# Kernel tuning notes

Hardware: AMD Instinct MI355X
Metric: run time of the kernel (lower is better)

Reference implementation:

```python
import jax, jax.numpy as jnp
import numpy as np

N = 27          # number of graph nodes (hardcoded in the module)
NH = 28         # n_hidden = out_features = self_size + 1
H = 8192        # n_heads
HA = 256        # num_hiddens_action
NO = 5          # num_outputs_action


def setup_inputs() -> dict:
    key = jax.random.key(0)
    ks = jax.random.split(key, 8)
    # node_embeddings: one_hot(node, 27) ++ reward flag (reward_nodes=[2] -> node index 1)
    node_emb = jnp.concatenate(
        [jnp.eye(N, dtype=jnp.float32),
         (jnp.arange(N) == 1).astype(jnp.float32)[:, None]], axis=1)  # [27,28]
    # adjacency [27,27,1], 0/1 ints, self-loops forced so softmax columns are valid
    adj = (jax.random.uniform(ks[0], (N, N, 1)) < 0.3).astype(jnp.int32)
    adj = adj.at[jnp.arange(N), jnp.arange(N), 0].set(1)
    # obs: one-hot current-location vector, node index 5 -> cur_node = 6
    obs = jnp.zeros((1, N), dtype=jnp.float32).at[0, 5].set(1.0)
    s = 0.02
    W_lin = jax.random.normal(ks[1], (N + 1, NH * H), dtype=jnp.float32) * s
    W_attn = jax.random.normal(ks[2], (2 * NH, 1), dtype=jnp.float32) * s
    b_attn = jax.random.normal(ks[3], (1,), dtype=jnp.float32) * s
    W1 = jax.random.normal(ks[4], (N + 1, HA), dtype=jnp.float32) * s
    b1 = jax.random.normal(ks[5], (HA,), dtype=jnp.float32) * s
    W2 = jax.random.normal(ks[6], (HA, NO), dtype=jnp.float32) * s
    b2 = jax.random.normal(ks[7], (NO,), dtype=jnp.float32) * s
    return {"obs": obs, "node_emb": node_emb, "adj": adj, "W_lin": W_lin,
            "W_attn": W_attn, "b_attn": b_attn, "W1": W1, "b1": b1,
            "W2": W2, "b2": b2}


def _leaky(x, slope):
    return jnp.where(x >= 0, x, slope * x)


def reference(obs, node_emb, adj, W_lin, W_attn, b_attn, W1, b1, W2, b2):
    # per-head projection: [27,28] @ [28, 28*8192] -> [27, H, NH]
    g = (node_emb @ W_lin).reshape(N, H, NH)
    # attn(concat(g_i, g_j)) decomposed: e[i,j,h] = g_i.Wl + g_j.Wr + b
    # (mathematically identical to the repeat/repeat_interleave + concat path,
    #  avoids materializing the [27,27,H,2*NH] tensor)
    Wl = W_attn[:NH, 0]
    Wr = W_attn[NH:, 0]
    s_i = jnp.einsum('nhf,f->nh', g, Wl)  # [N,H]
    s_j = jnp.einsum('nhf,f->nh', g, Wr)  # [N,H]
    e = _leaky(s_i[:, None, :] + s_j[None, :, :] + b_attn[0], 0.2)  # [N,N,H]
    # mask non-edges; adj [N,N,1] broadcasts over heads
    e = jnp.where(adj == 0, -jnp.inf, e)
    # torch nn.Softmax() with no dim resolves to dim=0 for 3-D input
    a = jax.nn.softmax(e, axis=0)
    # dropout is identity in eval mode
    attn_res = jnp.einsum('ijh,jhf->ihf', a, g)  # [N,H,NH]
    attn_res = attn_res.mean(axis=1)             # is_concat=False -> [N,NH]
    # cur_node = get_loc(bool obs) + 1; select attn_res[cur_node-1]
    idx = jnp.argmax(obs[0] != 0)
    x = attn_res[idx]                            # [NH]
    h = _leaky(x @ W1 + b1, 0.01)                # default LeakyReLU slope
    return h @ W2 + b2                           # [NO]
```

## Files before the change

### kernel.cpp

```cpp
#include <hip/hip_runtime.h>
#include <math.h>

#define NN 27
#define KD 28
#define HD 8192
#define HA_ 256
#define NO_ 5
#define NPAIR (KD*HD)
#define HB 32
#define NBLK (HD/HB)

__global__ void __launch_bounds__(256) kMain(const float* __restrict__ obs,
                                             const int* __restrict__ adj,
                                             const float* __restrict__ Wlin,
                                             const float* __restrict__ Wattn,
                                             const float* __restrict__ battn,
                                             float* __restrict__ ws) {
    __shared__ float P[HB][KD + 1];
    __shared__ float Q[HB][KD + 1];
    __shared__ float A[HB][KD];
    __shared__ unsigned adjm[NN];
    __shared__ float red[4][KD];

    const int t   = threadIdx.x;
    const int hl  = t >> 3;
    const int sub = t & 7;
    const int h   = blockIdx.x * HB + hl;

    if (t < NN) {
        unsigned m = 0;
        for (int i = 0; i < NN; ++i) m |= (adj[i * NN + t] != 0 ? 1u : 0u) << i;
        adjm[t] = m;
    }

    float wl[KD], wr[KD];
#pragma unroll
    for (int f = 0; f < KD; ++f) { wl[f] = Wattn[f]; wr[f] = Wattn[KD + f]; }

#pragma unroll
    for (int m = 0; m < 4; ++m) {
        int k = sub + 8 * m;
        if (k < KD) {
            const float4* w4 = reinterpret_cast<const float4*>(
                Wlin + (size_t)k * NPAIR + (size_t)h * KD);
            float p = 0.f, q = 0.f;
#pragma unroll
            for (int f4 = 0; f4 < 7; ++f4) {
                float4 w = w4[f4];
                p += w.x * wl[4*f4] + w.y * wl[4*f4+1] + w.z * wl[4*f4+2] + w.w * wl[4*f4+3];
                q += w.x * wr[4*f4] + w.y * wr[4*f4+1] + w.z * wr[4*f4+2] + w.w * wr[4*f4+3];
            }
            P[hl][k] = p;
            Q[hl][k] = q;
        }
    }
    __syncthreads();

    int idx = 0;
    for (int n = NN - 1; n >= 0; --n) if (obs[n] != 0.f) idx = n;
    const float bias = battn[0];

    float si[NN];
#pragma unroll
    for (int i = 0; i < NN; ++i)
        si[i] = P[hl][i] + (i == 1 ? P[hl][27] : 0.f) + bias;

#pragma unroll
    for (int m = 0; m < 4; ++m) {
        int j = sub + 8 * m;
        if (j < NN) {
            float sj = Q[hl][j] + (j == 1 ? Q[hl][27] : 0.f);
            unsigned msk = adjm[j];
            float ev[NN];
            float mx = -3.0e38f;
#pragma unroll
            for (int i = 0; i < NN; ++i) {
                float e = si[i] + sj;
                e = e >= 0.f ? e : 0.2f * e;
                ev[i] = e;
                if (((msk >> i) & 1) && e > mx) mx = e;
            }
            float den = 0.f, num = 0.f;
#pragma unroll
            for (int i = 0; i < NN; ++i) {
                float x = ((msk >> i) & 1) ? __expf(ev[i] - mx) : 0.f;
                den += x;
                if (i == idx) num = x;
            }
            A[hl][j] = num / den;
        }
    }
    __syncthreads();

    float acc[7][4];
#pragma unroll
    for (int f4 = 0; f4 < 7; ++f4)
#pragma unroll
        for (int c = 0; c < 4; ++c) acc[f4][c] = 0.f;

#pragma unroll
    for (int m = 0; m < 4; ++m) {
        int k = sub + 8 * m;
        if (k < KD) {
            float bk = (k < NN) ? A[hl][k] : A[hl][1];
            const float4* w4 = reinterpret_cast<const float4*>(
                Wlin + (size_t)k * NPAIR + (size_t)h * KD);
#pragma unroll
            for (int f4 = 0; f4 < 7; ++f4) {
                float4 w = w4[f4];
                acc[f4][0] += bk * w.x;
                acc[f4][1] += bk * w.y;
                acc[f4][2] += bk * w.z;
                acc[f4][3] += bk * w.w;
            }
        }
    }

#pragma unroll
    for (int off = 32; off > 0; off >>= 1)
#pragma unroll
        for (int f4 = 0; f4 < 7; ++f4)
#pragma unroll
            for (int c = 0; c < 4; ++c)
                acc[f4][c] += __shfl_xor(acc[f4][c], off, 64);

    const int lane = t & 63, wv = t >> 6;
    if (lane == 0) {
#pragma unroll
        for (int f4 = 0; f4 < 7; ++f4)
#pragma unroll
            for (int c = 0; c < 4; ++c) red[wv][f4 * 4 + c] = acc[f4][c];
    }
    __syncthreads();
    if (t < KD)
        ws[blockIdx.x * KD + t] = red[0][t] + red[1][t] + red[2][t] + red[3][t];
}

__global__ void __launch_bounds__(512) kF(const float* __restrict__ W1,
                                          const float* __restrict__ b1,
                                          const float* __restrict__ W2,
                                          const float* __restrict__ b2,
                                          const float* __restrict__ ws,
                                          float* __restrict__ out) {
    __shared__ float xp[KD][16];
    __shared__ float x[KD];
    __shared__ float hh[HA_];
    int t = threadIdx.x;
    int f = t >> 4, seg = t & 15;
    if (f < KD) {
        float s = 0.f;
        for (int b = seg; b < NBLK; b += 16) s += ws[b * KD + f];
        xp[f][seg] = s;
    }
    __syncthreads();
    if (t < KD) {
        float s = 0.f;
#pragma unroll
        for (int g = 0; g < 16; ++g) s += xp[t][g];
        x[t] = s * (1.0f / HD);
    }
    __syncthreads();
    if (t < HA_) {
        float s = b1[t];
#pragma unroll
        for (int k = 0; k < KD; ++k) s += x[k] * W1[k * HA_ + t];
        hh[t] = s >= 0.f ? s : 0.01f * s;
    }
    __syncthreads();
    if (t < NO_) {
        float s = b2[t];
        for (int u = 0; u < HA_; ++u) s += hh[u] * W2[u * NO_ + t];
        out[t] = s;
    }
}

extern "C" void kernel_launch(void* const* d_in, const int* in_sizes, int n_in,
                              void* d_out, int out_size, void* d_ws, size_t ws_size,
                              hipStream_t stream) {
    const float* obs   = (const float*)d_in[0];
    const int*   adj   = (const int*)  d_in[2];
    const float* Wlin  = (const float*)d_in[3];
    const float* Wattn = (const float*)d_in[4];
    const float* battn = (const float*)d_in[5];
    const float* W1    = (const float*)d_in[6];
    const float* b1    = (const float*)d_in[7];
    const float* W2    = (const float*)d_in[8];
    const float* b2    = (const float*)d_in[9];
    float* ws  = (float*)d_ws;
    float* out = (float*)d_out;

    kMain<<<NBLK, 256, 0, stream>>>(obs, adj, Wlin, Wattn, battn, ws);
    kF<<<1, 512, 0, stream>>>(W1, b1, W2, b2, ws, out);
}
```

Before: 29.25 us.

## Shrink heads per block and map one thread per feature row to keep weights in registers

The heads per block drop from 32 to 8 and threads are remapped so each thread loads exactly one 28-float row of W_lin once, keeping it in registers for both the score pass and the weighted-sum pass. Previously each row was read from global memory twice. Softmax work is now spread across 216 threads, one per (head, j) pair, instead of looping. The grid becomes four times larger (1024 blocks), so the final reduction kernel sums four times more partials and the per-block shuffle reductions add overhead. Coalescing also changes, since 8 consecutive threads now read adjacent heads.

Result: slower. 30.17 us (+3.1%).

```diff
diff --git a/kernel.cpp b/kernel.cpp
--- a/kernel.cpp
+++ b/kernel.cpp
@@ -7,25 +7,26 @@
 #define HA_ 256
 #define NO_ 5
 #define NPAIR (KD*HD)
-#define HB 32
+#define HB 8
 #define NBLK (HD/HB)
 
-__global__ void __launch_bounds__(256) kMain(const float* __restrict__ obs,
-                                             const int* __restrict__ adj,
-                                             const float* __restrict__ Wlin,
-                                             const float* __restrict__ Wattn,
-                                             const float* __restrict__ battn,
-                                             float* __restrict__ ws) {
+
+__global__ void __launch_bounds__(256, 4) kMain(const float* __restrict__ obs,
+                                                const int* __restrict__ adj,
+                                                const float* __restrict__ Wlin,
+                                                const float* __restrict__ Wattn,
+                                                const float* __restrict__ battn,
+                                                float* __restrict__ ws) {
     __shared__ float P[HB][KD + 1];
     __shared__ float Q[HB][KD + 1];
     __shared__ float A[HB][KD];
     __shared__ unsigned adjm[NN];
     __shared__ float red[4][KD];
 
-    const int t   = threadIdx.x;
-    const int hl  = t >> 3;
-    const int sub = t & 7;
-    const int h   = blockIdx.x * HB + hl;
+    const int t  = threadIdx.x;
+    const int k  = t >> 3;
+    const int hl = t & 7;
+    const int h  = blockIdx.x * HB + hl;
 
     if (t < NN) {
         unsigned m = 0;
@@ -33,103 +34,77 @@
         adjm[t] = m;
     }
 
-    float wl[KD], wr[KD];
+    float4 wv[7];
+    if (k < KD) {
+        const float4* src = reinterpret_cast<const float4*>(
+            Wlin + (size_t)k * NPAIR + (size_t)h * KD);
+        const float4* wl4 = reinterpret_cast<const float4*>(Wattn);
+        const float4* wr4 = reinterpret_cast<const float4*>(Wattn + KD);
 #pragma unroll
-    for (int f = 0; f < KD; ++f) { wl[f] = Wattn[f]; wr[f] = Wattn[KD + f]; }
-
+        for (int f4 = 0; f4 < 7; ++f4) wv[f4] = src[f4];
+        float p = 0.f, q = 0.f;
 #pragma unroll
-    for (int m = 0; m < 4; ++m) {
-        int k = sub + 8 * m;
-        if (k < KD) {
-            const float4* w4 = reinterpret_cast<const float4*>(
-                Wlin + (size_t)k * NPAIR + (size_t)h * KD);
-            float p = 0.f, q = 0.f;
-#pragma unroll
-            for (int f4 = 0; f4 < 7; ++f4) {
-                float4 w = w4[f4];
-                p += w.x * wl[4*f4] + w.y * wl[4*f4+1] + w.z * wl[4*f4+2] + w.w * wl[4*f4+3];
-                q += w.x * wr[4*f4] + w.y * wr[4*f4+1] + w.z * wr[4*f4+2] + w.w * wr[4*f4+3];
-            }
-            P[hl][k] = p;
-            Q[hl][k] = q;
+        for (int f4 = 0; f4 < 7; ++f4) {
+            float4 wl = wl4[f4], wr = wr4[f4], w = wv[f4];
+            p += w.x * wl.x + w.y * wl.y + w.z * wl.z + w.w * wl.w;
+            q += w.x * wr.x + w.y * wr.y + w.z * wr.z + w.w * wr.w;
         }
+        P[hl][k] = p;
+        Q[hl][k] = q;
     }
     __syncthreads();
 
-    int idx = 0;
-    for (int n = NN - 1; n >= 0; --n) if (obs[n] != 0.f) idx = n;
-    const float bias = battn[0];
-
-    float si[NN];
+    if (t < HB * NN) {
+        const int hl2 = t / NN, j = t - hl2 * NN;
+        int idx = 0;
+        for (int n = NN - 1; n >= 0; --n) if (obs[n] != 0.f) idx = n;
+        const float bias = battn[0];
+        const float p27 = P[hl2][27], q27 = Q[hl2][27];
+        const float sj = Q[hl2][j] + (j == 1 ? q27 : 0.f) + bias;
+        const unsigned msk = adjm[j];
+        float mx = -3.0e38f;
 #pragma unroll
-    for (int i = 0; i < NN; ++i)
-        si[i] = P[hl][i] + (i == 1 ? P[hl][27] : 0.f) + bias;
-
+        for (int i = 0; i < NN; ++i) {
+            float e = P[hl2][i] + (i == 1 ? p27 : 0.f) + sj;
+            e = e >= 0.f ? e : 0.2f * e;
+            if (((msk >> i) & 1) && e > mx) mx = e;
+        }
+        float den = 0.f, num = 0.f;
 #pragma unroll
-    for (int m = 0; m < 4; ++m) {
-        int j = sub + 8 * m;
-        if (j < NN) {
-            float sj = Q[hl][j] + (j == 1 ? Q[hl][27] : 0.f);
-            unsigned msk = adjm[j];
-            float ev[NN];
-            float mx = -3.0e38f;
-#pragma unroll
-            for (int i = 0; i < NN; ++i) {
-                float e = si[i] + sj;
-                e = e >= 0.f ? e : 0.2f * e;
-                ev[i] = e;
-                if (((msk >> i) & 1) && e > mx) mx = e;
-            }
-            float den = 0.f, num = 0.f;
-#pragma unroll
-            for (int i = 0; i < NN; ++i) {
-                float x = ((msk >> i) & 1) ? __expf(ev[i] - mx) : 0.f;
-                den += x;
-                if (i == idx) num = x;
-            }
-            A[hl][j] = num / den;
+        for (int i = 0; i < NN; ++i) {
+            float e = P[hl2][i] + (i == 1 ? p27 : 0.f) + sj;
+            e = e >= 0.f ? e : 0.2f * e;
+            float x = ((msk >> i) & 1) ? __expf(e - mx) : 0.f;
+            den += x;
+            if (i == idx) num = x;
         }
+        A[hl2][j] = num / den;
     }
     __syncthreads();
 
-    float acc[7][4];
+    float acc[KD];
+    if (k < KD) {
+        const float bk = A[hl][k < NN ? k : 1];
 #pragma unroll
-    for (int f4 = 0; f4 < 7; ++f4)
+        for (int f4 = 0; f4 < 7; ++f4) {
+            acc[4*f4+0] = bk * wv[f4].x;
+            acc[4*f4+1] = bk * wv[f4].y;
+            acc[4*f4+2] = bk * wv[f4].z;
+            acc[4*f4+3] = bk * wv[f4].w;
+        }
+    } else {
 #pragma unroll
-        for (int c = 0; c < 4; ++c) acc[f4][c] = 0.f;
-
-#pragma unroll
-    for (int m = 0; m < 4; ++m) {
-        int k = sub + 8 * m;
-        if (k < KD) {
-            float bk = (k < NN) ? A[hl][k] : A[hl][1];
-            const float4* w4 = reinterpret_cast<const float4*>(
-                Wlin + (size_t)k * NPAIR + (size_t)h * KD);
-#pragma unroll
-            for (int f4 = 0; f4 < 7; ++f4) {
-                float4 w = w4[f4];
-                acc[f4][0] += bk * w.x;
-                acc[f4][1] += bk * w.y;
-                acc[f4][2] += bk * w.z;
-                acc[f4][3] += bk * w.w;
-            }
-        }
+        for (int f = 0; f < KD; ++f) acc[f] = 0.f;
     }
-
 #pragma unroll
     for (int off = 32; off > 0; off >>= 1)
 #pragma unroll
-        for (int f4 = 0; f4 < 7; ++f4)
-#pragma unroll
-            for (int c = 0; c < 4; ++c)
-                acc[f4][c] += __shfl_xor(acc[f4][c], off, 64);
+        for (int f = 0; f < KD; ++f) acc[f] += __shfl_xor(acc[f], off, 64);
 
-    const int lane = t & 63, wv = t >> 6;
+    const int lane = t & 63, wv_id = t >> 6;
     if (lane == 0) {
 #pragma unroll
-        for (int f4 = 0; f4 < 7; ++f4)
-#pragma unroll
-            for (int c = 0; c < 4; ++c) red[wv][f4 * 4 + c] = acc[f4][c];
+        for (int f = 0; f < KD; ++f) red[wv_id][f] = acc[f];
     }
     __syncthreads();
     if (t < KD)
@@ -145,10 +120,11 @@
     __shared__ float xp[KD][16];
     __shared__ float x[KD];
     __shared__ float hh[HA_];
-    int t = threadIdx.x;
-    int f = t >> 4, seg = t & 15;
-    if (f < KD) {
+    const int t = threadIdx.x;
+    if (t < 16 * KD) {
+        const int seg = t / KD, f = t - seg * KD;
         float s = 0.f;
+#pragma unroll 4
         for (int b = seg; b < NBLK; b += 16) s += ws[b * KD + f];
         xp[f][seg] = s;
     }
@@ -163,7 +139,7 @@
     if (t < HA_) {
         float s = b1[t];
 #pragma unroll
-        for (int k = 0; k < KD; ++k) s += x[k] * W1[k * HA_ + t];
+        for (int kk = 0; kk < KD; ++kk) s += x[kk] * W1[kk * HA_ + t];
         hh[t] = s >= 0.f ? s : 0.01f * s;
     }
     __syncthreads();
```
